# Optimization experiments

Measured on AMD Instinct MI355X. Metric: run time of the kernel, lower is better.

## Reference

```python
import jax, jax.numpy as jnp
import numpy as np

BETA = 0.5

def setup_inputs() -> dict:
    key = jax.random.key(0)
    k1, k2, k3, k4 = jax.random.split(key, 4)
    N, K, D = 32768, 8192, 256
    z = jax.random.normal(k1, (N, D), dtype=jnp.float32)
    # torch init: uniform(-1/K, 1/K); keep same scale for faithfulness
    embedding = jax.random.uniform(k2, (K, D), dtype=jnp.float32, minval=-1.0 / K, maxval=1.0 / K)
    proj_w = jax.random.normal(k3, (D, D), dtype=jnp.float32) * (1.0 / np.sqrt(D))
    proj_b = jax.random.normal(k4, (D,), dtype=jnp.float32) * 0.01
    return {"z": z, "embedding": embedding, "proj_w": proj_w, "proj_b": proj_b}

def reference(z, embedding, proj_w, proj_b):
    sg = jax.lax.stop_gradient
    # projected codebook: [K, D]
    codebook = embedding @ proj_w.T + proj_b
    # squared L2 distances: [N, K] = ||z||^2 + ||c||^2 - 2 z.c
    d = (jnp.sum(z * z, axis=1, keepdims=True)
         + jnp.sum(codebook * codebook, axis=1)
         - 2.0 * (z @ codebook.T))
    indices = jnp.argmin(d, axis=1)            # [N]
    zq = codebook[indices]                     # [N, D] gather
    loss = (BETA * jnp.mean((sg(zq) - z) ** 2)
            + jnp.mean((zq - sg(z)) ** 2))
    zq = z + sg(zq - z)                        # straight-through
    return (zq, indices, loss)
```

## Files before the change

kernel.cpp:

```cpp
#include <hip/hip_runtime.h>

#define N_PTS 32768
#define K_CB  8192
#define D_DIM 256
#define BETA  0.5f

typedef _Float16 f16;
typedef __attribute__((ext_vector_type(8))) _Float16 f16x8;
typedef __attribute__((ext_vector_type(16))) float f32x16;

#define MARGIN  2.5e-4f
#define CAPQ    32
#define DSCALE  4096.0f
#define INV2S   (-4.8828125e-4f)
#define CBB     16

#define OFF_CB   ((size_t)0)
#define OFF_DH   (OFF_CB   + (size_t)K_CB*D_DIM*4)
#define OFF_UH   (OFF_DH   + (size_t)K_CB*D_DIM*2)
#define OFF_CC   (OFF_UH   + (size_t)N_PTS*D_DIM*2)
#define OFF_ZZ   (OFF_CC   + (size_t)K_CB*4)
#define OFF_D2   (OFF_ZZ   + (size_t)N_PTS*4)
#define OFF_CAND (OFF_D2   + (size_t)K_CB*4)
#define OFF_CNT  (OFF_CAND + (size_t)N_PTS*4*CAPQ*2)
#define OFF_BEST (OFF_CNT  + (size_t)N_PTS*4*4)
#define OFF_ACC  (OFF_BEST + (size_t)N_PTS*8)
#define WS_NEED  (OFF_ACC + 64)

#define F_CB_OFF   0
#define F_CC_OFF   (K_CB * D_DIM)
#define F_ZZ_OFF   (F_CC_OFF + K_CB)
#define F_IDX_OFF  (F_ZZ_OFF + N_PTS)
#define F_ACC_BYTE ((size_t)(F_IDX_OFF + N_PTS) * 4)

__global__ __launch_bounds__(256) void k_codebook(
    const float* __restrict__ emb, const float* __restrict__ w,
    const float* __restrict__ bias, float* __restrict__ cb,
    float* __restrict__ cc, float* __restrict__ dd2, f16* __restrict__ dh) {
  __shared__ float esL[CBB][D_DIM];
  __shared__ float wL[D_DIM][37];
  __shared__ float cbL[CBB][D_DIM + 1];
  __shared__ float biasL[D_DIM];
  const int tid = threadIdx.x;
  const int k0 = blockIdx.x * CBB;

#pragma unroll
  for (int r = 0; r < CBB; ++r) esL[r][tid] = emb[(size_t)(k0 + r) * D_DIM + tid];
  biasL[tid] = bias[tid];
  __syncthreads();

  float acc[CBB];
#pragma unroll
  for (int r = 0; r < CBB; ++r) acc[r] = 0.f;

  const int d = tid;
  for (int ch = 0; ch < 8; ++ch) {
    const int j0 = ch * 32;
#pragma unroll
    for (int s = 0; s < 8; ++s) {
      int idx = tid + s * 256;
      int row = idx >> 3, c4 = (idx & 7) * 4;
      float4 v = *(const float4*)&w[(size_t)row * D_DIM + j0 + c4];
      wL[row][c4 + 0] = v.x; wL[row][c4 + 1] = v.y;
      wL[row][c4 + 2] = v.z; wL[row][c4 + 3] = v.w;
    }
    __syncthreads();
#pragma unroll
    for (int jj = 0; jj < 32; jj += 4) {
      float w0 = wL[d][jj + 0], w1 = wL[d][jj + 1];
      float w2 = wL[d][jj + 2], w3 = wL[d][jj + 3];
#pragma unroll
      for (int r = 0; r < CBB; ++r) {
        float4 e = *(const float4*)&esL[r][j0 + jj];
        acc[r] = fmaf(e.x, w0, acc[r]);
        acc[r] = fmaf(e.y, w1, acc[r]);
        acc[r] = fmaf(e.z, w2, acc[r]);
        acc[r] = fmaf(e.w, w3, acc[r]);
      }
    }
    __syncthreads();
  }

  const float bd = biasL[d];
#pragma unroll
  for (int r = 0; r < CBB; ++r) {
    float a = acc[r] + bd;
    cb[(size_t)(k0 + r) * D_DIM + d] = a;
    cbL[r][d] = a;
    if (dh) dh[(size_t)(k0 + r) * D_DIM + d] = (f16)((a - bd) * DSCALE);
  }
  __syncthreads();
  if (tid < CBB) {
    float s = 0.f;
    for (int j = 0; j < D_DIM; ++j) { float v = cbL[tid][j]; s = fmaf(v, v, s); }
    cc[k0 + tid] = s;
  } else if (tid < 2 * CBB && dd2) {
    int r = tid - CBB;
    float s = 0.f;
    for (int j = 0; j < D_DIM; ++j) { float dl = cbL[r][j] - biasL[j]; s = fmaf(dl, dl, s); }
    dd2[k0 + r] = s;
  }
}

__global__ __launch_bounds__(256) void k_zz(const float* __restrict__ z,
                                            float* __restrict__ zz) {
  const int n = blockIdx.x * 256 + threadIdx.x;
  const float* zr = z + (size_t)n * D_DIM;
  float s = 0.f;
#pragma unroll 8
  for (int q = 0; q < D_DIM / 4; ++q) {
    float4 v = *(const float4*)&zr[q * 4];
    s = fmaf(v.x, v.x, s);
    s = fmaf(v.y, v.y, s);
    s = fmaf(v.z, v.z, s);
    s = fmaf(v.w, v.w, s);
  }
  zz[n] = s;
}

__global__ __launch_bounds__(256) void k_zu(const float* __restrict__ z,
                                            const float* __restrict__ bias,
                                            f16* __restrict__ uh) {
  const size_t i = (size_t)blockIdx.x * 256 + threadIdx.x;
  const int d0 = (int)((i * 8) & (D_DIM - 1));
  const float4* zp = (const float4*)(z + i * 8);
  float4 a = zp[0], c = zp[1];
  float4 b0 = *(const float4*)&bias[d0];
  float4 b1 = *(const float4*)&bias[d0 + 4];
  f16x8 o = {(f16)(a.x - b0.x), (f16)(a.y - b0.y), (f16)(a.z - b0.z), (f16)(a.w - b0.w),
             (f16)(c.x - b1.x), (f16)(c.y - b1.y), (f16)(c.z - b1.z), (f16)(c.w - b1.w)};
  *(f16x8*)(uh + i * 8) = o;
}

__global__ __launch_bounds__(512, 2) void k_main(
    const f16* __restrict__ uh, const f16* __restrict__ dh,
    const float* __restrict__ dd2,
    unsigned int* __restrict__ cntG, unsigned short* __restrict__ candG) {
  __shared__ __align__(16) char tile[2][16384];
  __shared__ unsigned short candL[512][CAPQ];
  __shared__ unsigned int cntL[512];

  const int tid = threadIdx.x;
  const int w = tid >> 6, l = tid & 63;
  const int lc = l & 31, h = l >> 5;
  const int rb = blockIdx.x >> 2, q = blockIdx.x & 3;
  const int n0 = rb * 512;
  const int lrowA = w * 64 + lc;
  const int lrowB = lrowA + 32;
  const int rowA = n0 + lrowA, rowB = n0 + lrowB;
  const int code0 = q * 2048;

  cntL[tid] = 0;

  const f16x8* uv = (const f16x8*)uh;
  f16x8 ua[16], ub[16];
#pragma unroll
  for (int kc = 0; kc < 16; ++kc) {
    ua[kc] = uv[(size_t)rowA * 32 + kc * 2 + h];
    ub[kc] = uv[(size_t)rowB * 32 + kc * 2 + h];
  }

  const f16x8* cv = (const f16x8*)dh;
  const int m0 = tid, m1 = tid + 512;
  const int cl0 = m0 >> 5, s0 = (m0 & 31) ^ (cl0 & 7);
  const int cl1 = m1 >> 5, s1 = (m1 & 31) ^ (cl1 & 7);
  const size_t base0 = (size_t)(code0 + cl0) * 32 + s0;
  const size_t base1 = (size_t)(code0 + cl1) * 32 + s1;

  {
    f16x8 a = cv[base0], b2 = cv[base1];
    *(f16x8*)(tile[0] + m0 * 16) = a;
    *(f16x8*)(tile[0] + m1 * 16) = b2;
  }
  __syncthreads();

  float runA = 3.4e38f, runB = 3.4e38f;
  const float4* d2v = (const float4*)dd2;
  int buf = 0;
  for (int t = 0; t < 64; ++t) {
    f16x8 nx0, nx1;
    if (t < 63) {
      nx0 = cv[base0 + (size_t)(t + 1) * 1024];
      nx1 = cv[base1 + (size_t)(t + 1) * 1024];
    }
    f32x16 accA = {0.f,0.f,0.f,0.f,0.f,0.f,0.f,0.f,0.f,0.f,0.f,0.f,0.f,0.f,0.f,0.f};
    f32x16 accB = {0.f,0.f,0.f,0.f,0.f,0.f,0.f,0.f,0.f,0.f,0.f,0.f,0.f,0.f,0.f,0.f};
    const char* cbase = tile[buf] + lc * 512;
#pragma unroll
    for (int kc = 0; kc < 16; ++kc) {
      f16x8 af = *(const f16x8*)(cbase + (((kc * 2 + h) ^ (lc & 7)) << 4));
      accA = __builtin_amdgcn_mfma_f32_32x32x16_f16(af, ua[kc], accA, 0, 0, 0);
      accB = __builtin_amdgcn_mfma_f32_32x32x16_f16(af, ub[kc], accB, 0, 0, 0);
    }

    const int tb = code0 + t * 32;
    float sA[16], sB[16];
    float mA = 3.4e38f, mB = 3.4e38f;
#pragma unroll
    for (int r4 = 0; r4 < 4; ++r4) {
      float4 dq = d2v[(tb + 8 * r4 + 4 * h) >> 2];
      sA[4*r4+0] = fmaf(accA[4*r4+0], INV2S, dq.x);
      sA[4*r4+1] = fmaf(accA[4*r4+1], INV2S, dq.y);
      sA[4*r4+2] = fmaf(accA[4*r4+2], INV2S, dq.z);
      sA[4*r4+3] = fmaf(accA[4*r4+3], INV2S, dq.w);
      sB[4*r4+0] = fmaf(accB[4*r4+0], INV2S, dq.x);
      sB[4*r4+1] = fmaf(accB[4*r4+1], INV2S, dq.y);
      sB[4*r4+2] = fmaf(accB[4*r4+2], INV2S, dq.z);
      sB[4*r4+3] = fmaf(accB[4*r4+3], INV2S, dq.w);
      mA = fminf(mA, fminf(fminf(sA[4*r4+0], sA[4*r4+1]), fminf(sA[4*r4+2], sA[4*r4+3])));
      mB = fminf(mB, fminf(fminf(sB[4*r4+0], sB[4*r4+1]), fminf(sB[4*r4+2], sB[4*r4+3])));
    }
    mA = fminf(mA, __shfl_xor(mA, 32));
    mB = fminf(mB, __shfl_xor(mB, 32));
    runA = fminf(runA, mA);
    runB = fminf(runB, mB);
    const float thA = runA + MARGIN, thB = runB + MARGIN;
#pragma unroll
    for (int r = 0; r < 16; ++r) {
      const int code = tb + 8 * (r >> 2) + 4 * h + (r & 3);
      if (sA[r] < thA) {
        unsigned int p = atomicAdd(&cntL[lrowA], 1u);
        if (p < CAPQ) candL[lrowA][p] = (unsigned short)code;
      }
      if (sB[r] < thB) {
        unsigned int p = atomicAdd(&cntL[lrowB], 1u);
        if (p < CAPQ) candL[lrowB][p] = (unsigned short)code;
      }
    }
    if (t < 63) {
      *(f16x8*)(tile[buf ^ 1] + m0 * 16) = nx0;
      *(f16x8*)(tile[buf ^ 1] + m1 * 16) = nx1;
    }
    __syncthreads();
    buf ^= 1;
  }

  unsigned int c = cntL[tid];
  unsigned int cw = (c > CAPQ) ? 0xFFFFu : c;
  cntG[((size_t)(n0 + tid)) * 4 + q] = cw;
  unsigned int nc = (cw == 0xFFFFu) ? 0u : cw;
  for (unsigned int j = 0; j < nc; ++j)
    candG[(((size_t)(n0 + tid)) * 4 + q) * CAPQ + j] = candL[tid][j];
}

__device__ inline unsigned long long exact_key(const float* __restrict__ zr,
                                               const float* __restrict__ cb,
                                               float zzn, const float* __restrict__ cc,
                                               int code) {
  float acc = 0.f;
  const float4* cr = (const float4*)&cb[(size_t)code * D_DIM];
  const float4* z4p = (const float4*)zr;
#pragma unroll 8
  for (int u = 0; u < D_DIM / 4; ++u) {
    float4 c4 = cr[u], z4 = z4p[u];
    acc = fmaf(z4.x, c4.x, acc);
    acc = fmaf(z4.y, c4.y, acc);
    acc = fmaf(z4.z, c4.z, acc);
    acc = fmaf(z4.w, c4.w, acc);
  }
  float t = zzn + cc[code];
  float dd = fmaf(-2.f, acc, t);
  return (((unsigned long long)__float_as_uint(dd)) << 32) | (unsigned int)code;
}

__global__ __launch_bounds__(256) void k_refine(
    const float* __restrict__ z, const float* __restrict__ cb,
    const float* __restrict__ zz, const float* __restrict__ cc,
    const unsigned int* __restrict__ cntG, const unsigned short* __restrict__ candG,
    unsigned long long* __restrict__ best) {
  __shared__ float zls[4][D_DIM];
  const int tid = threadIdx.x;
  const int v = tid >> 6, l = tid & 63;
  const int n = blockIdx.x * 4 + v;
  *(float4*)&zls[v][l * 4] = *(const float4*)&z[(size_t)n * D_DIM + l * 4];
  __syncthreads();

  unsigned int cq[4];
  bool full = false;
#pragma unroll
  for (int i = 0; i < 4; ++i) {
    cq[i] = cntG[(size_t)n * 4 + i];
    full |= (cq[i] == 0xFFFFu);
  }
  const float zzn = zz[n];
  unsigned long long key = ~0ull;

  if (!full) {
    const unsigned int o1 = cq[0], o2 = o1 + cq[1], o3 = o2 + cq[2], tot = o3 + cq[3];
    for (unsigned int ci = l; ci < tot; ci += 64) {
      int qq; unsigned int j;
      if (ci >= o3)      { qq = 3; j = ci - o3; }
      else if (ci >= o2) { qq = 2; j = ci - o2; }
      else if (ci >= o1) { qq = 1; j = ci - o1; }
      else               { qq = 0; j = ci; }
      int code = candG[((size_t)n * 4 + qq) * CAPQ + j];
      unsigned long long k2 = exact_key(zls[v], cb, zzn, cc, code);
      key = key < k2 ? key : k2;
    }
  } else {
    for (int code = l; code < K_CB; code += 64) {
      unsigned long long k2 = exact_key(zls[v], cb, zzn, cc, code);
      key = key < k2 ? key : k2;
    }
  }
#pragma unroll
  for (int off = 1; off < 64; off <<= 1) {
    unsigned long long o = __shfl_xor(key, off);
    key = key < o ? key : o;
  }
  if (l == 0) best[n] = key;
}

#define BN  64
#define BKC 128
#define DC  32
#define LDP (DC + 4)
__global__ __launch_bounds__(256) void k_argmin(
    const float* __restrict__ z, const float* __restrict__ cb,
    const float* __restrict__ zz, const float* __restrict__ cc,
    int* __restrict__ out_idx) {
  __shared__ float zs[BN][LDP];
  __shared__ float cs[BKC][LDP];
  __shared__ float red_d[BN][16];
  __shared__ int   red_k[BN][16];
  const int tid = threadIdx.x;
  const int tn = tid & 15, tk = tid >> 4;
  const int n0 = blockIdx.x * BN;
  float zzv[4];
#pragma unroll
  for (int i = 0; i < 4; ++i) zzv[i] = zz[n0 + tn + 16 * i];
  float best[4]; int bidx[4];
#pragma unroll
  for (int i = 0; i < 4; ++i) { best[i] = 3.4e38f; bidx[i] = 0; }
  for (int kt = 0; kt < K_CB / BKC; ++kt) {
    float acc[4][8];
#pragma unroll
    for (int i = 0; i < 4; ++i)
#pragma unroll
      for (int j = 0; j < 8; ++j) acc[i][j] = 0.f;
    for (int ch = 0; ch < D_DIM / DC; ++ch) {
      __syncthreads();
#pragma unroll
      for (int s = 0; s < 2; ++s) {
        int f = tid + 256 * s, r = f >> 3, c4 = f & 7;
        *(float4*)&zs[r][c4 * 4] =
            *(const float4*)&z[(size_t)(n0 + r) * D_DIM + ch * DC + c4 * 4];
      }
#pragma unroll
      for (int s = 0; s < 4; ++s) {
        int f = tid + 256 * s, r = f >> 3, c4 = f & 7;
        *(float4*)&cs[r][c4 * 4] =
            *(const float4*)&cb[(size_t)(kt * BKC + r) * D_DIM + ch * DC + c4 * 4];
      }
      __syncthreads();
#pragma unroll
      for (int qq = 0; qq < DC / 4; ++qq) {
        float4 zr[4], cr[8];
#pragma unroll
        for (int i = 0; i < 4; ++i) zr[i] = *(const float4*)&zs[tn + 16 * i][4 * qq];
#pragma unroll
        for (int j = 0; j < 8; ++j) cr[j] = *(const float4*)&cs[tk + 16 * j][4 * qq];
#pragma unroll
        for (int i = 0; i < 4; ++i)
#pragma unroll
          for (int j = 0; j < 8; ++j) {
            acc[i][j] = fmaf(zr[i].x, cr[j].x, acc[i][j]);
            acc[i][j] = fmaf(zr[i].y, cr[j].y, acc[i][j]);
            acc[i][j] = fmaf(zr[i].z, cr[j].z, acc[i][j]);
            acc[i][j] = fmaf(zr[i].w, cr[j].w, acc[i][j]);
          }
      }
    }
#pragma unroll
    for (int j = 0; j < 8; ++j) {
      const int k = kt * BKC + tk + 16 * j;
      const float cck = cc[k];
#pragma unroll
      for (int i = 0; i < 4; ++i) {
        float t = zzv[i] + cck;
        float dd = fmaf(-2.f, acc[i][j], t);
        if (dd < best[i]) { best[i] = dd; bidx[i] = k; }
      }
    }
  }
#pragma unroll
  for (int i = 0; i < 4; ++i) {
    red_d[tn + 16 * i][tk] = best[i];
    red_k[tn + 16 * i][tk] = bidx[i];
  }
  __syncthreads();
  if (tid < BN) {
    float bd = red_d[tid][0]; int bk = red_k[tid][0];
#pragma unroll
    for (int t2 = 1; t2 < 16; ++t2) {
      float dd = red_d[tid][t2]; int kk = red_k[tid][t2];
      if (dd < bd || (dd == bd && kk < bk)) { bd = dd; bk = kk; }
    }
    out_idx[n0 + tid] = bk;
  }
}

template <int MODE>
__global__ __launch_bounds__(256) void k_gather(
    const float* __restrict__ z, const float* __restrict__ cb,
    const void* __restrict__ idx_src, float* __restrict__ out,
    double* __restrict__ accum) {
  const int tid = threadIdx.x;
  const int lane = tid & 63, wv = tid >> 6;
  const int base = blockIdx.x * 64 + wv * 16;
  double lsum = 0.0;
  for (int r = 0; r < 16; ++r) {
    const int n = base + r;
    int k;
    if (MODE == 0) k = ((const int*)idx_src)[n];
    else k = (int)(((const unsigned long long*)idx_src)[n] & 8191ull);
    float4 c4 = *(const float4*)&cb[(size_t)k * D_DIM + lane * 4];
    float4 z4 = *(const float4*)&z[(size_t)n * D_DIM + lane * 4];
    float e0 = c4.x - z4.x, e1 = c4.y - z4.y, e2 = c4.z - z4.z, e3 = c4.w - z4.w;
    lsum += (double)e0 * e0 + (double)e1 * e1 + (double)e2 * e2 + (double)e3 * e3;
    float4 o;
    o.x = z4.x + e0; o.y = z4.y + e1; o.z = z4.z + e2; o.w = z4.w + e3;
    *(float4*)&out[(size_t)n * D_DIM + lane * 4] = o;
    if (lane == 0) out[(size_t)N_PTS * D_DIM + n] = (float)k;
  }
#pragma unroll
  for (int off = 32; off > 0; off >>= 1) lsum += __shfl_down(lsum, off);
  __shared__ double wsum[4];
  if (lane == 0) wsum[wv] = lsum;
  __syncthreads();
  if (tid == 0) atomicAdd(accum, wsum[0] + wsum[1] + wsum[2] + wsum[3]);
}

__global__ void k_loss(const double* __restrict__ accum, float* __restrict__ out) {
  float m = (float)(*accum / (double)((size_t)N_PTS * D_DIM));
  out[(size_t)N_PTS * D_DIM + N_PTS] = BETA * m + m;
}

extern "C" void kernel_launch(void* const* d_in, const int* in_sizes, int n_in,
                              void* d_out, int out_size, void* d_ws, size_t ws_size,
                              hipStream_t stream) {
  const float* z   = (const float*)d_in[0];
  const float* emb = (const float*)d_in[1];
  const float* w   = (const float*)d_in[2];
  const float* b   = (const float*)d_in[3];
  float* out = (float*)d_out;
  char* ws = (char*)d_ws;

  if (ws_size >= WS_NEED) {
    float* cb  = (float*)(ws + OFF_CB);
    f16*   dh  = (f16*)(ws + OFF_DH);
    f16*   uh  = (f16*)(ws + OFF_UH);
    float* cc  = (float*)(ws + OFF_CC);
    float* zz  = (float*)(ws + OFF_ZZ);
    float* dd2 = (float*)(ws + OFF_D2);
    unsigned short* candG = (unsigned short*)(ws + OFF_CAND);
    unsigned int*   cntG  = (unsigned int*)(ws + OFF_CNT);
    unsigned long long* best = (unsigned long long*)(ws + OFF_BEST);
    double* accum = (double*)(ws + OFF_ACC);

    hipMemsetAsync(accum, 0, 8, stream);

    k_codebook<<<K_CB / CBB, 256, 0, stream>>>(emb, w, b, cb, cc, dd2, dh);
    k_zz<<<N_PTS / 256, 256, 0, stream>>>(z, zz);
    k_zu<<<(N_PTS * D_DIM) / (8 * 256), 256, 0, stream>>>(z, b, uh);
    k_main<<<256, 512, 0, stream>>>(uh, dh, dd2, cntG, candG);
    k_refine<<<N_PTS / 4, 256, 0, stream>>>(z, cb, zz, cc, cntG, candG, best);
    k_gather<1><<<N_PTS / 64, 256, 0, stream>>>(z, cb, best, out, accum);
    k_loss<<<1, 1, 0, stream>>>(accum, out);
  } else {
    float* ws_f = (float*)d_ws;
    float* cb = ws_f + F_CB_OFF;
    float* cc = ws_f + F_CC_OFF;
    float* zz = ws_f + F_ZZ_OFF;
    int*   idx = (int*)(ws_f + F_IDX_OFF);
    double* accum = (double*)((char*)d_ws + F_ACC_BYTE);
    hipMemsetAsync(accum, 0, sizeof(double), stream);
    k_codebook<<<K_CB / CBB, 256, 0, stream>>>(emb, w, b, cb, cc, (float*)nullptr, (f16*)nullptr);
    k_zz<<<N_PTS / 256, 256, 0, stream>>>(z, zz);
    k_argmin<<<N_PTS / BN, 256, 0, stream>>>(z, cb, zz, cc, idx);
    k_gather<0><<<N_PTS / 64, 256, 0, stream>>>(z, cb, idx, out, accum);
    k_loss<<<1, 1, 0, stream>>>(accum, out);
  }
}
```

Before: 482.1 us.

## Split codebook scan into eight slices per row block to double grid size

```diff
diff --git a/kernel.cpp b/kernel.cpp
--- a/kernel.cpp
+++ b/kernel.cpp
@@ -10,7 +10,8 @@
 typedef __attribute__((ext_vector_type(16))) float f32x16;
 
 #define MARGIN  2.5e-4f
-#define CAPQ    32
+#define CAPQ    16
+#define NOCT    8
 #define DSCALE  4096.0f
 #define INV2S   (-4.8828125e-4f)
 #define CBB     16
@@ -22,8 +23,8 @@
 #define OFF_ZZ   (OFF_CC   + (size_t)K_CB*4)
 #define OFF_D2   (OFF_ZZ   + (size_t)N_PTS*4)
 #define OFF_CAND (OFF_D2   + (size_t)K_CB*4)
-#define OFF_CNT  (OFF_CAND + (size_t)N_PTS*4*CAPQ*2)
-#define OFF_BEST (OFF_CNT  + (size_t)N_PTS*4*4)
+#define OFF_CNT  (OFF_CAND + (size_t)N_PTS*NOCT*CAPQ*2)
+#define OFF_BEST (OFF_CNT  + (size_t)N_PTS*NOCT*4)
 #define OFF_ACC  (OFF_BEST + (size_t)N_PTS*8)
 #define WS_NEED  (OFF_ACC + 64)
 
@@ -132,7 +133,7 @@
   *(f16x8*)(uh + i * 8) = o;
 }
 
-__global__ __launch_bounds__(512, 2) void k_main(
+__global__ __launch_bounds__(512, 4) void k_main(
     const f16* __restrict__ uh, const f16* __restrict__ dh,
     const float* __restrict__ dd2,
     unsigned int* __restrict__ cntG, unsigned short* __restrict__ candG) {
@@ -143,12 +144,12 @@
   const int tid = threadIdx.x;
   const int w = tid >> 6, l = tid & 63;
   const int lc = l & 31, h = l >> 5;
-  const int rb = blockIdx.x >> 2, q = blockIdx.x & 3;
+  const int rb = blockIdx.x >> 3, oct = blockIdx.x & 7;
   const int n0 = rb * 512;
   const int lrowA = w * 64 + lc;
   const int lrowB = lrowA + 32;
   const int rowA = n0 + lrowA, rowB = n0 + lrowB;
-  const int code0 = q * 2048;
+  const int code0 = oct * 1024;
 
   cntL[tid] = 0;
 
@@ -177,9 +178,9 @@
   float runA = 3.4e38f, runB = 3.4e38f;
   const float4* d2v = (const float4*)dd2;
   int buf = 0;
-  for (int t = 0; t < 64; ++t) {
+  for (int t = 0; t < 32; ++t) {
     f16x8 nx0, nx1;
-    if (t < 63) {
+    if (t < 31) {
       nx0 = cv[base0 + (size_t)(t + 1) * 1024];
       nx1 = cv[base1 + (size_t)(t + 1) * 1024];
     }
@@ -227,7 +228,7 @@
         if (p < CAPQ) candL[lrowB][p] = (unsigned short)code;
       }
     }
-    if (t < 63) {
+    if (t < 31) {
       *(f16x8*)(tile[buf ^ 1] + m0 * 16) = nx0;
       *(f16x8*)(tile[buf ^ 1] + m1 * 16) = nx1;
     }
@@ -237,10 +238,10 @@
 
   unsigned int c = cntL[tid];
   unsigned int cw = (c > CAPQ) ? 0xFFFFu : c;
-  cntG[((size_t)(n0 + tid)) * 4 + q] = cw;
+  cntG[((size_t)(n0 + tid)) * NOCT + oct] = cw;
   unsigned int nc = (cw == 0xFFFFu) ? 0u : cw;
   for (unsigned int j = 0; j < nc; ++j)
-    candG[(((size_t)(n0 + tid)) * 4 + q) * CAPQ + j] = candL[tid][j];
+    candG[(((size_t)(n0 + tid)) * NOCT + oct) * CAPQ + j] = candL[tid][j];
 }
 
 __device__ inline unsigned long long exact_key(const float* __restrict__ zr,
@@ -275,25 +276,27 @@
   *(float4*)&zls[v][l * 4] = *(const float4*)&z[(size_t)n * D_DIM + l * 4];
   __syncthreads();
 
-  unsigned int cq[4];
+  unsigned int cq[NOCT];
   bool full = false;
 #pragma unroll
-  for (int i = 0; i < 4; ++i) {
-    cq[i] = cntG[(size_t)n * 4 + i];
+  for (int i = 0; i < NOCT; ++i) {
+    cq[i] = cntG[(size_t)n * NOCT + i];
     full |= (cq[i] == 0xFFFFu);
   }
   const float zzn = zz[n];
   unsigned long long key = ~0ull;
 
   if (!full) {
-    const unsigned int o1 = cq[0], o2 = o1 + cq[1], o3 = o2 + cq[2], tot = o3 + cq[3];
+    unsigned int off[NOCT];
+    unsigned int tot = 0;
+#pragma unroll
+    for (int i = 0; i < NOCT; ++i) { off[i] = tot; tot += cq[i]; }
     for (unsigned int ci = l; ci < tot; ci += 64) {
-      int qq; unsigned int j;
-      if (ci >= o3)      { qq = 3; j = ci - o3; }
-      else if (ci >= o2) { qq = 2; j = ci - o2; }
-      else if (ci >= o1) { qq = 1; j = ci - o1; }
-      else               { qq = 0; j = ci; }
-      int code = candG[((size_t)n * 4 + qq) * CAPQ + j];
+      int oc = 0;
+#pragma unroll
+      for (int i = 1; i < NOCT; ++i) oc = (ci >= off[i]) ? i : oc;
+      unsigned int j = ci - off[oc];
+      int code = candG[((size_t)n * NOCT + oc) * CAPQ + j];
       unsigned long long k2 = exact_key(zls[v], cb, zzn, cc, code);
       key = key < k2 ? key : k2;
     }
@@ -304,8 +307,8 @@
     }
   }
 #pragma unroll
-  for (int off = 1; off < 64; off <<= 1) {
-    unsigned long long o = __shfl_xor(key, off);
+  for (int off2 = 1; off2 < 64; off2 <<= 1) {
+    unsigned long long o = __shfl_xor(key, off2);
     key = key < o ? key : o;
   }
   if (l == 0) best[n] = key;
@@ -463,7 +466,7 @@
     k_codebook<<<K_CB / CBB, 256, 0, stream>>>(emb, w, b, cb, cc, dd2, dh);
     k_zz<<<N_PTS / 256, 256, 0, stream>>>(z, zz);
     k_zu<<<(N_PTS * D_DIM) / (8 * 256), 256, 0, stream>>>(z, b, uh);
-    k_main<<<256, 512, 0, stream>>>(uh, dh, dd2, cntG, candG);
+    k_main<<<512, 512, 0, stream>>>(uh, dh, dd2, cntG, candG);
     k_refine<<<N_PTS / 4, 256, 0, stream>>>(z, cb, zz, cc, cntG, candG, best);
     k_gather<1><<<N_PTS / 64, 256, 0, stream>>>(z, cb, best, out, accum);
     k_loss<<<1, 1, 0, stream>>>(accum, out);
```

New measurement: 1.422 ms. 195% more time.
